# Kernel optimization log

Hardware: AMD Instinct MI355X
Metric: run time of the kernel (lower is better)

The kernel has to match this reference:

```python
import jax, jax.numpy as jnp
import numpy as np

HC = 4
C = 256
TMAX = 20
RMS_EPS = 1e-6
PRE_EPS = 0.0
SINKHORN_EPS = 1e-6
POST_MULT = 2.0


def setup_inputs() -> dict:
    key = jax.random.key(0)
    k1, k2, k3 = jax.random.split(key, 3)
    B, S = 8, 4096
    m = HC * HC + 2 * HC
    x = jax.random.normal(k1, (B, S, HC, C), dtype=jnp.float32)
    phi = jax.random.normal(k2, (HC * C, m), dtype=jnp.float32) * 0.02
    b = jnp.zeros((m,), dtype=jnp.float32)
    W = jax.random.normal(k3, (C, C), dtype=jnp.float32) * (1.0 / np.sqrt(C))
    return {
        "x": x, "phi": phi, "b": b,
        "alpha_pre": jnp.float32(1.0), "alpha_post": jnp.float32(1.0), "alpha_res": jnp.float32(1.0),
        "W": W,
    }


def _mhc_coeffs(x, phi, b, alpha_pre, alpha_post, alpha_res):
    # x: [..., HC, C] -> flatten streams, project, RMS-normalize logits.
    lead = x.shape[:-2]
    v = x.reshape(lead + (HC * C,))
    logits = jnp.einsum('...k,km->...m', v, phi)            # [..., m]
    rms = jnp.sqrt(jnp.mean(logits * logits, axis=-1, keepdims=True) + RMS_EPS)
    y = logits / rms + b                                     # [..., m]
    pre = y[..., :HC]
    post = y[..., HC:2 * HC]
    res = y[..., 2 * HC:].reshape(lead + (HC, HC))
    h_pre = jax.nn.sigmoid(alpha_pre * pre) + PRE_EPS        # [..., HC]
    h_post = POST_MULT * jax.nn.sigmoid(alpha_post * post)   # [..., HC]
    # Sinkhorn-Knopp: make exp(alpha_res * res) approximately doubly stochastic.
    P = jnp.exp(alpha_res * res)                             # [..., HC, HC]

    def step(P, _):
        P = P / (jnp.sum(P, axis=-1, keepdims=True) + SINKHORN_EPS)  # row norm
        P = P / (jnp.sum(P, axis=-2, keepdims=True) + SINKHORN_EPS)  # col norm
        return P, None

    P, _ = jax.lax.scan(step, P, None, length=TMAX)
    return h_pre, h_post, P


def reference(x, phi, b, alpha_pre, alpha_post, alpha_res, W):
    h_pre, h_post, h_res = _mhc_coeffs(x, phi, b, alpha_pre, alpha_post, alpha_res)
    # Pre-aggregate streams: x_in = sum_i h_pre[i] * x[i]
    x_in = jnp.einsum('...i,...ic->...c', h_pre, x)          # [..., C]
    # Wrapped layer: nn.Linear(C, C, bias=False) -> x_in @ W.T
    f_out = x_in @ W.T                                       # [..., C]
    # Post + residual: x_out[o] = sum_i h_res[o,i]*x[i] + h_post[o]*f_out
    x_out = jnp.einsum('...oi,...ic->...oc', h_res, x) + h_post[..., :, None] * f_out[..., None, :]
    return x_out
```

## Files before the change

### kernel.cpp

```cpp
#include <hip/hip_runtime.h>

typedef __attribute__((ext_vector_type(4))) float floatx4;
typedef __attribute__((ext_vector_type(8))) short short8;

__device__ __forceinline__ unsigned short f2bf(float f) {
    union { float f; unsigned int i; } v; v.f = f;
    unsigned int x = v.i;
    unsigned int r = (x + 0x7FFFu + ((x >> 16) & 1u)) >> 16;
    return (unsigned short)r;
}
__device__ __forceinline__ float bf2f(unsigned short u) {
    union { unsigned int i; float f; } v; v.i = ((unsigned int)u) << 16;
    return v.f;
}

__device__ __forceinline__ unsigned int cvtpk_bf16(float lo, float hi) {
    unsigned int r;
    asm("v_cvt_pk_bf16_f32 %0, %1, %2" : "=v"(r) : "v"(lo), "v"(hi));
    return r;
}

template<int CTRL>
__device__ __forceinline__ float dppf(float x) {
    return __int_as_float(__builtin_amdgcn_update_dpp(
        0, __float_as_int(x), CTRL, 0xF, 0xF, false));
}

__global__ void mhc_prep(const float* __restrict__ phi, const float* __restrict__ W,
                         unsigned short* __restrict__ phiF, unsigned short* __restrict__ WF) {
    int e = blockIdx.x * 256 + threadIdx.x;
    if (e < 32768) {
        int j = e & 7, lane = (e >> 3) & 63, nt = (e >> 9) & 1, ks = e >> 10;
        int n = nt * 16 + (lane & 15);
        int k = ks * 32 + ((lane >> 4) & 3) * 8 + j;
        float v = (n < 24) ? phi[k * 24 + n] : 0.0f;
        phiF[e] = f2bf(v);
    } else {
        int e2 = e - 32768;
        int j = e2 & 7, lane = (e2 >> 3) & 63, ks = (e2 >> 9) & 7, nt = e2 >> 12;
        int n = nt * 16 + (lane & 15);
        int k = ks * 32 + ((lane >> 4) & 3) * 8 + j;
        WF[e2] = f2bf(W[n * 256 + k]);
    }
}

#define XS_STRIDE 1032
#define CO_STRIDE 28

__global__ __launch_bounds__(256) void mhc_coef(
    const float* __restrict__ x, const float* __restrict__ bias,
    const float* __restrict__ s_ap, const float* __restrict__ s_apo,
    const float* __restrict__ s_ar,
    const unsigned short* __restrict__ phiF,
    float* __restrict__ cbuf)
{
    __shared__ unsigned short xs[16 * XS_STRIDE];
    __shared__ float lgp[2][16 * CO_STRIDE];

    const int t = threadIdx.x;
    const int lane = t & 63;
    const int w = t >> 6;
    const int quad = lane >> 4;
    const int col = lane & 15;
    const long base = (long)blockIdx.x * (16 * 1024);

    {
        const float4* xg = (const float4*)(x + base);
        #pragma unroll
        for (int ii = 0; ii < 16; ++ii) {
            int lin = ii * 256 + t;
            float4 v = xg[lin];
            int tok = lin >> 8;
            int k = (lin & 255) * 4;
            uint2 pk;
            pk.x = cvtpk_bf16(v.x, v.y);
            pk.y = cvtpk_bf16(v.z, v.w);
            *reinterpret_cast<uint2*>(&xs[tok * XS_STRIDE + k]) = pk;
        }
    }
    __syncthreads();

    {
        floatx4 acc = {0.0f, 0.0f, 0.0f, 0.0f};
        const int ntile = w & 1;
        const int kh = w >> 1;
        for (int ks = kh * 16; ks < kh * 16 + 16; ++ks) {
            short8 a = *reinterpret_cast<const short8*>(&xs[col * XS_STRIDE + ks * 32 + quad * 8]);
            short8 b = *reinterpret_cast<const short8*>(&phiF[(ks * 2 + ntile) * 512 + lane * 8]);
            acc = __builtin_amdgcn_mfma_f32_16x16x32_bf16(a, b, acc, 0, 0, 0);
        }
        int n = ntile * 16 + col;
        if (n < 24) {
            #pragma unroll
            for (int r = 0; r < 4; ++r)
                lgp[kh][(quad * 4 + r) * CO_STRIDE + n] = acc[r];
        }
    }
    __syncthreads();

    {
        int g = t >> 4, p = t & 15;
        float a  = lgp[0][g * CO_STRIDE + p]      + lgp[1][g * CO_STRIDE + p];
        float b2 = (p < 8) ? (lgp[0][g * CO_STRIDE + 16 + p] + lgp[1][g * CO_STRIDE + 16 + p]) : 0.0f;
        float s = a * a + b2 * b2;
        s += dppf<0x121>(s);
        s += dppf<0x122>(s);
        s += dppf<0x124>(s);
        s += dppf<0x128>(s);
        float rinv = 1.0f / sqrtf(s * (1.0f / 24.0f) + 1e-6f);
        float lr = lgp[0][g * CO_STRIDE + 8 + p] + lgp[1][g * CO_STRIDE + 8 + p];
        float yP = lr * rinv + bias[8 + p];
        float P = expf(s_ar[0] * yP);
        for (int it = 0; it < 20; ++it) {
            float r = P + dppf<0x39>(P);
            r += dppf<0x4E>(r);
            P *= __builtin_amdgcn_rcpf(r + 1e-6f);
            float c = P + dppf<0x124>(P);
            c += dppf<0x128>(c);
            P *= __builtin_amdgcn_rcpf(c + 1e-6f);
        }
        long tok = (long)blockIdx.x * 16 + g;
        cbuf[tok * 24 + 8 + p] = P;
        if (p < 8) {
            float yh = a * rinv + bias[p];
            float h = (p < 4) ? 1.0f / (1.0f + expf(-s_ap[0] * yh))
                              : 2.0f / (1.0f + expf(-s_apo[0] * yh));
            cbuf[tok * 24 + p] = h;
        }
    }
}

#define XIN_STRIDE 264

__global__ __launch_bounds__(256) void mhc_apply(
    const float* __restrict__ x, const float* __restrict__ cbuf,
    const unsigned short* __restrict__ WF, float* __restrict__ out)
{
    __shared__ unsigned short xin[16 * XIN_STRIDE];
    __shared__ float coef[16 * 24];

    const int t = threadIdx.x;
    const int lane = t & 63;
    const int w = t >> 6;
    const int quad = lane >> 4;
    const int col = lane & 15;
    const long base = (long)blockIdx.x * (16 * 1024);

    {
        const float* cg = cbuf + (long)blockIdx.x * 384;
        coef[t] = cg[t];
        if (t < 128) coef[256 + t] = cg[256 + t];
    }
    __syncthreads();

    {
        const float* xb = x + base + t;
        #pragma unroll 4
        for (int tok = 0; tok < 16; ++tok) {
            float4 h4 = *reinterpret_cast<const float4*>(&coef[tok * 24]);
            const float* xr = xb + tok * 1024;
            float s = h4.x * xr[0] + h4.y * xr[256] + h4.z * xr[512] + h4.w * xr[768];
            xin[tok * XIN_STRIDE + t] = f2bf(s);
        }
    }
    __syncthreads();

    short8 afr[8];
    #pragma unroll
    for (int ks = 0; ks < 8; ++ks)
        afr[ks] = *reinterpret_cast<const short8*>(&xin[col * XIN_STRIDE + ks * 32 + quad * 8]);
    floatx4 accs[4];
    #pragma unroll
    for (int nt = 0; nt < 4; ++nt) {
        floatx4 acc = {0.0f, 0.0f, 0.0f, 0.0f};
        int ntile = w * 4 + nt;
        #pragma unroll
        for (int ks = 0; ks < 8; ++ks) {
            short8 b = *reinterpret_cast<const short8*>(&WF[(ntile * 8 + ks) * 512 + lane * 8]);
            acc = __builtin_amdgcn_mfma_f32_16x16x32_bf16(afr[ks], b, acc, 0, 0, 0);
        }
        accs[nt] = acc;
    }

    #pragma unroll
    for (int r = 0; r < 4; ++r) {
        int tok = quad * 4 + r;
        const float* cb = &coef[tok * 24];
        float4 hpo = *reinterpret_cast<const float4*>(cb + 4);
        float4 P0  = *reinterpret_cast<const float4*>(cb + 8);
        float4 P1  = *reinterpret_cast<const float4*>(cb + 12);
        float4 P2  = *reinterpret_cast<const float4*>(cb + 16);
        float4 P3  = *reinterpret_cast<const float4*>(cb + 20);
        long ob = base + (long)tok * 1024;
        const float* xr0 = x + ob;
        #pragma unroll
        for (int nt = 0; nt < 4; ++nt) {
            int c = (w * 4 + nt) * 16 + col;
            float f = accs[nt][r];
            float x0 = xr0[c],       x1 = xr0[256 + c];
            float x2 = xr0[512 + c], x3 = xr0[768 + c];
            out[ob + c]       = P0.x * x0 + P0.y * x1 + P0.z * x2 + P0.w * x3 + hpo.x * f;
            out[ob + 256 + c] = P1.x * x0 + P1.y * x1 + P1.z * x2 + P1.w * x3 + hpo.y * f;
            out[ob + 512 + c] = P2.x * x0 + P2.y * x1 + P2.z * x2 + P2.w * x3 + hpo.z * f;
            out[ob + 768 + c] = P3.x * x0 + P3.y * x1 + P3.z * x2 + P3.w * x3 + hpo.w * f;
        }
    }
}

extern "C" void kernel_launch(void* const* d_in, const int* in_sizes, int n_in,
                              void* d_out, int out_size, void* d_ws, size_t ws_size,
                              hipStream_t stream) {
    const float* x    = (const float*)d_in[0];
    const float* phi  = (const float*)d_in[1];
    const float* bias = (const float*)d_in[2];
    const float* ap   = (const float*)d_in[3];
    const float* apo  = (const float*)d_in[4];
    const float* ar   = (const float*)d_in[5];
    const float* W    = (const float*)d_in[6];
    float* out = (float*)d_out;

    unsigned short* phiF = (unsigned short*)d_ws;
    unsigned short* WF   = (unsigned short*)d_ws + 32768;
    float* cbuf = (float*)((char*)d_ws + 196608);

    mhc_prep<<<384, 256, 0, stream>>>(phi, W, phiF, WF);
    mhc_coef<<<2048, 256, 0, stream>>>(x, bias, ap, apo, ar, phiF, cbuf);
    mhc_apply<<<2048, 256, 0, stream>>>(x, cbuf, WF, out);
}
```

Measured before the change: 284.2 us.

## Fuse coefficient and apply kernels into one kernel with 8 tokens per block

```diff
diff --git a/kernel.cpp b/kernel.cpp
--- a/kernel.cpp
+++ b/kernel.cpp
@@ -8,10 +8,6 @@
     unsigned int x = v.i;
     unsigned int r = (x + 0x7FFFu + ((x >> 16) & 1u)) >> 16;
     return (unsigned short)r;
-}
-__device__ __forceinline__ float bf2f(unsigned short u) {
-    union { unsigned int i; float f; } v; v.i = ((unsigned int)u) << 16;
-    return v.f;
 }
 
 __device__ __forceinline__ unsigned int cvtpk_bf16(float lo, float hi) {
@@ -44,38 +40,41 @@
     }
 }
 
+#define TOK 8
 #define XS_STRIDE 1032
+#define XIN_STRIDE 264
 #define CO_STRIDE 28
-
-__global__ __launch_bounds__(256) void mhc_coef(
+#define F_STRIDE 260
+
+__global__ __launch_bounds__(256, 7) void mhc_main(
     const float* __restrict__ x, const float* __restrict__ bias,
     const float* __restrict__ s_ap, const float* __restrict__ s_apo,
     const float* __restrict__ s_ar,
-    const unsigned short* __restrict__ phiF,
-    float* __restrict__ cbuf)
+    const unsigned short* __restrict__ phiF, const unsigned short* __restrict__ WF,
+    float* __restrict__ out)
 {
-    __shared__ unsigned short xs[16 * XS_STRIDE];
-    __shared__ float lgp[2][16 * CO_STRIDE];
+    __shared__ alignas(16) unsigned short xs[TOK * XS_STRIDE];
+    __shared__ alignas(16) unsigned short xin[TOK * XIN_STRIDE];
+    __shared__ alignas(16) float lgp[2][TOK * CO_STRIDE];
+    __shared__ alignas(16) float coef[TOK * 24];
+    float* fbuf = reinterpret_cast<float*>(xs);
 
     const int t = threadIdx.x;
     const int lane = t & 63;
     const int w = t >> 6;
     const int quad = lane >> 4;
     const int col = lane & 15;
-    const long base = (long)blockIdx.x * (16 * 1024);
+    const long base = (long)blockIdx.x * (TOK * 1024);
 
     {
         const float4* xg = (const float4*)(x + base);
         #pragma unroll
-        for (int ii = 0; ii < 16; ++ii) {
-            int lin = ii * 256 + t;
-            float4 v = xg[lin];
-            int tok = lin >> 8;
-            int k = (lin & 255) * 4;
+        for (int ii = 0; ii < TOK; ++ii) {
+            float4 v = xg[ii * 256 + t];
             uint2 pk;
             pk.x = cvtpk_bf16(v.x, v.y);
             pk.y = cvtpk_bf16(v.z, v.w);
-            *reinterpret_cast<uint2*>(&xs[tok * XS_STRIDE + k]) = pk;
+            *reinterpret_cast<uint2*>(&xs[ii * XS_STRIDE + t * 4]) = pk;
         }
     }
     __syncthreads();
@@ -84,13 +83,14 @@
         floatx4 acc = {0.0f, 0.0f, 0.0f, 0.0f};
         const int ntile = w & 1;
         const int kh = w >> 1;
+        const int arow = col & 7;
         for (int ks = kh * 16; ks < kh * 16 + 16; ++ks) {
-            short8 a = *reinterpret_cast<const short8*>(&xs[col * XS_STRIDE + ks * 32 + quad * 8]);
+            short8 a = *reinterpret_cast<const short8*>(&xs[arow * XS_STRIDE + ks * 32 + quad * 8]);
             short8 b = *reinterpret_cast<const short8*>(&phiF[(ks * 2 + ntile) * 512 + lane * 8]);
             acc = __builtin_amdgcn_mfma_f32_16x16x32_bf16(a, b, acc, 0, 0, 0);
         }
         int n = ntile * 16 + col;
-        if (n < 24) {
+        if (n < 24 && quad < 2) {
             #pragma unroll
             for (int r = 0; r < 4; ++r)
                 lgp[kh][(quad * 4 + r) * CO_STRIDE + n] = acc[r];
@@ -98,7 +98,7 @@
     }
     __syncthreads();
 
-    {
+    if (t < 128) {
         int g = t >> 4, p = t & 15;
         float a  = lgp[0][g * CO_STRIDE + p]      + lgp[1][g * CO_STRIDE + p];
         float b2 = (p < 8) ? (lgp[0][g * CO_STRIDE + 16 + p] + lgp[1][g * CO_STRIDE + 16 + p]) : 0.0f;
@@ -119,90 +119,111 @@
             c += dppf<0x128>(c);
             P *= __builtin_amdgcn_rcpf(c + 1e-6f);
         }
-        long tok = (long)blockIdx.x * 16 + g;
-        cbuf[tok * 24 + 8 + p] = P;
+        coef[g * 24 + 8 + p] = P;
         if (p < 8) {
             float yh = a * rinv + bias[p];
             float h = (p < 4) ? 1.0f / (1.0f + expf(-s_ap[0] * yh))
                               : 2.0f / (1.0f + expf(-s_apo[0] * yh));
-            cbuf[tok * 24 + p] = h;
-        }
-    }
-}
-
-#define XIN_STRIDE 264
-
-__global__ __launch_bounds__(256) void mhc_apply(
-    const float* __restrict__ x, const float* __restrict__ cbuf,
-    const unsigned short* __restrict__ WF, float* __restrict__ out)
-{
-    __shared__ unsigned short xin[16 * XIN_STRIDE];
-    __shared__ float coef[16 * 24];
-
-    const int t = threadIdx.x;
-    const int lane = t & 63;
-    const int w = t >> 6;
-    const int quad = lane >> 4;
-    const int col = lane & 15;
-    const long base = (long)blockIdx.x * (16 * 1024);
-
-    {
-        const float* cg = cbuf + (long)blockIdx.x * 384;
-        coef[t] = cg[t];
-        if (t < 128) coef[256 + t] = cg[256 + t];
-    }
-    __syncthreads();
-
-    {
-        const float* xb = x + base + t;
-        #pragma unroll 4
-        for (int tok = 0; tok < 16; ++tok) {
+            coef[g * 24 + p] = h;
+        }
+    }
+    __syncthreads();
+
+    {
+        const int cc = (t & 63) * 4;
+        const int tok0 = w * 2;
+        #pragma unroll
+        for (int s = 0; s < 2; ++s) {
+            int tok = tok0 + s;
             float4 h4 = *reinterpret_cast<const float4*>(&coef[tok * 24]);
-            const float* xr = xb + tok * 1024;
-            float s = h4.x * xr[0] + h4.y * xr[256] + h4.z * xr[512] + h4.w * xr[768];
-            xin[tok * XIN_STRIDE + t] = f2bf(s);
-        }
-    }
-    __syncthreads();
-
-    short8 afr[8];
-    #pragma unroll
-    for (int ks = 0; ks < 8; ++ks)
-        afr[ks] = *reinterpret_cast<const short8*>(&xin[col * XIN_STRIDE + ks * 32 + quad * 8]);
-    floatx4 accs[4];
-    #pragma unroll
-    for (int nt = 0; nt < 4; ++nt) {
-        floatx4 acc = {0.0f, 0.0f, 0.0f, 0.0f};
-        int ntile = w * 4 + nt;
-        #pragma unroll
-        for (int ks = 0; ks < 8; ++ks) {
-            short8 b = *reinterpret_cast<const short8*>(&WF[(ntile * 8 + ks) * 512 + lane * 8]);
-            acc = __builtin_amdgcn_mfma_f32_16x16x32_bf16(afr[ks], b, acc, 0, 0, 0);
-        }
-        accs[nt] = acc;
-    }
-
-    #pragma unroll
-    for (int r = 0; r < 4; ++r) {
-        int tok = quad * 4 + r;
-        const float* cb = &coef[tok * 24];
-        float4 hpo = *reinterpret_cast<const float4*>(cb + 4);
-        float4 P0  = *reinterpret_cast<const float4*>(cb + 8);
-        float4 P1  = *reinterpret_cast<const float4*>(cb + 12);
-        float4 P2  = *reinterpret_cast<const float4*>(cb + 16);
-        float4 P3  = *reinterpret_cast<const float4*>(cb + 20);
-        long ob = base + (long)tok * 1024;
-        const float* xr0 = x + ob;
+            const float* xr = x + base + tok * 1024 + cc;
+            float4 x0 = *reinterpret_cast<const float4*>(xr);
+            float4 x1 = *reinterpret_cast<const float4*>(xr + 256);
+            float4 x2 = *reinterpret_cast<const float4*>(xr + 512);
+            float4 x3 = *reinterpret_cast<const float4*>(xr + 768);
+            float4 sr;
+            sr.x = h4.x * x0.x + h4.y * x1.x + h4.z * x2.x + h4.w * x3.x;
+            sr.y = h4.x * x0.y + h4.y * x1.y + h4.z * x2.y + h4.w * x3.y;
+            sr.z = h4.x * x0.z + h4.y * x1.z + h4.z * x2.z + h4.w * x3.z;
+            sr.w = h4.x * x0.w + h4.y * x1.w + h4.z * x2.w + h4.w * x3.w;
+            uint2 pk;
+            pk.x = cvtpk_bf16(sr.x, sr.y);
+            pk.y = cvtpk_bf16(sr.z, sr.w);
+            *reinterpret_cast<uint2*>(&xin[tok * XIN_STRIDE + cc]) = pk;
+        }
+    }
+    __syncthreads();
+
+    {
+        const int arow = col & 7;
+        short8 afr[8];
+        #pragma unroll
+        for (int ks = 0; ks < 8; ++ks)
+            afr[ks] = *reinterpret_cast<const short8*>(&xin[arow * XIN_STRIDE + ks * 32 + quad * 8]);
+        floatx4 accs[4];
         #pragma unroll
         for (int nt = 0; nt < 4; ++nt) {
-            int c = (w * 4 + nt) * 16 + col;
-            float f = accs[nt][r];
-            float x0 = xr0[c],       x1 = xr0[256 + c];
-            float x2 = xr0[512 + c], x3 = xr0[768 + c];
-            out[ob + c]       = P0.x * x0 + P0.y * x1 + P0.z * x2 + P0.w * x3 + hpo.x * f;
-            out[ob + 256 + c] = P1.x * x0 + P1.y * x1 + P1.z * x2 + P1.w * x3 + hpo.y * f;
-            out[ob + 512 + c] = P2.x * x0 + P2.y * x1 + P2.z * x2 + P2.w * x3 + hpo.z * f;
-            out[ob + 768 + c] = P3.x * x0 + P3.y * x1 + P3.z * x2 + P3.w * x3 + hpo.w * f;
+            floatx4 acc = {0.0f, 0.0f, 0.0f, 0.0f};
+            int ntile = w * 4 + nt;
+            #pragma unroll
+            for (int ks = 0; ks < 8; ++ks) {
+                short8 b = *reinterpret_cast<const short8*>(&WF[(ntile * 8 + ks) * 512 + lane * 8]);
+                acc = __builtin_amdgcn_mfma_f32_16x16x32_bf16(afr[ks], b, acc, 0, 0, 0);
+            }
+            accs[nt] = acc;
+        }
+        if (quad < 2) {
+            #pragma unroll
+            for (int nt = 0; nt < 4; ++nt) {
+                int n = (w * 4 + nt) * 16 + col;
+                #pragma unroll
+                for (int r = 0; r < 4; ++r)
+                    fbuf[(quad * 4 + r) * F_STRIDE + n] = accs[nt][r];
+            }
+        }
+    }
+    __syncthreads();
+
+    {
+        const int cc = (t & 63) * 4;
+        const int tok0 = w * 2;
+        #pragma unroll
+        for (int s = 0; s < 2; ++s) {
+            int tok = tok0 + s;
+            const float* cb = &coef[tok * 24];
+            float4 hpo = *reinterpret_cast<const float4*>(cb + 4);
+            float4 P0  = *reinterpret_cast<const float4*>(cb + 8);
+            float4 P1  = *reinterpret_cast<const float4*>(cb + 12);
+            float4 P2  = *reinterpret_cast<const float4*>(cb + 16);
+            float4 P3  = *reinterpret_cast<const float4*>(cb + 20);
+            const float* xr = x + base + tok * 1024 + cc;
+            float4 x0 = *reinterpret_cast<const float4*>(xr);
+            float4 x1 = *reinterpret_cast<const float4*>(xr + 256);
+            float4 x2 = *reinterpret_cast<const float4*>(xr + 512);
+            float4 x3 = *reinterpret_cast<const float4*>(xr + 768);
+            float4 f  = *reinterpret_cast<const float4*>(&fbuf[tok * F_STRIDE + cc]);
+            float* ob = out + base + tok * 1024 + cc;
+            float4 o0, o1, o2, o3;
+            o0.x = P0.x*x0.x + P0.y*x1.x + P0.z*x2.x + P0.w*x3.x + hpo.x*f.x;
+            o0.y = P0.x*x0.y + P0.y*x1.y + P0.z*x2.y + P0.w*x3.y + hpo.x*f.y;
+            o0.z = P0.x*x0.z + P0.y*x1.z + P0.z*x2.z + P0.w*x3.z + hpo.x*f.z;
+            o0.w = P0.x*x0.w + P0.y*x1.w + P0.z*x2.w + P0.w*x3.w + hpo.x*f.w;
+            o1.x = P1.x*x0.x + P1.y*x1.x + P1.z*x2.x + P1.w*x3.x + hpo.y*f.x;
+            o1.y = P1.x*x0.y + P1.y*x1.y + P1.z*x2.y + P1.w*x3.y + hpo.y*f.y;
+            o1.z = P1.x*x0.z + P1.y*x1.z + P1.z*x2.z + P1.w*x3.z + hpo.y*f.z;
+            o1.w = P1.x*x0.w + P1.y*x1.w + P1.z*x2.w + P1.w*x3.w + hpo.y*f.w;
+            o2.x = P2.x*x0.x + P2.y*x1.x + P2.z*x2.x + P2.w*x3.x + hpo.z*f.x;
+            o2.y = P2.x*x0.y + P2.y*x1.y + P2.z*x2.y + P2.w*x3.y + hpo.z*f.y;
+            o2.z = P2.x*x0.z + P2.y*x1.z + P2.z*x2.z + P2.w*x3.z + hpo.z*f.z;
+            o2.w = P2.x*x0.w + P2.y*x1.w + P2.z*x2.w + P2.w*x3.w + hpo.z*f.w;
+            o3.x = P3.x*x0.x + P3.y*x1.x + P3.z*x2.x + P3.w*x3.x + hpo.w*f.x;
+            o3.y = P3.x*x0.y + P3.y*x1.y + P3.z*x2.y + P3.w*x3.y + hpo.w*f.y;
+            o3.z = P3.x*x0.z + P3.y*x1.z + P3.z*x2.z + P3.w*x3.z + hpo.w*f.z;
+            o3.w = P3.x*x0.w + P3.y*x1.w + P3.z*x2.w + P3.w*x3.w + hpo.w*f.w;
+            *reinterpret_cast<float4*>(ob)       = o0;
+            *reinterpret_cast<float4*>(ob + 256) = o1;
+            *reinterpret_cast<float4*>(ob + 512) = o2;
+            *reinterpret_cast<float4*>(ob + 768) = o3;
         }
     }
 }
@@ -221,9 +242,7 @@
 
     unsigned short* phiF = (unsigned short*)d_ws;
     unsigned short* WF   = (unsigned short*)d_ws + 32768;
-    float* cbuf = (float*)((char*)d_ws + 196608);
 
     mhc_prep<<<384, 256, 0, stream>>>(phi, W, phiF, WF);
-    mhc_coef<<<2048, 256, 0, stream>>>(x, bias, ap, apo, ar, phiF, cbuf);
-    mhc_apply<<<2048, 256, 0, stream>>>(x, cbuf, WF, out);
-}
+    mhc_main<<<4096, 256, 0, stream>>>(x, bias, ap, apo, ar, phiF, WF, out);
+}
```

Result: faster. 274.4 us (-3.5%).
